# Kernel tuning notes

Hardware: AMD Instinct MI355X
Metric: run time of the kernel (lower is better)

The kernel has to match this reference:

```python
import jax, jax.numpy as jnp
import numpy as np

N_HEAD = 16
D_HEAD = 64
D_MODEL = 1024
LN_EPS = 1e-5


def layer_norm(x, gamma, beta):
    mu = jnp.mean(x, axis=-1, keepdims=True)
    var = jnp.mean((x - mu) ** 2, axis=-1, keepdims=True)
    return (x - mu) * jax.lax.rsqrt(var + LN_EPS) * gamma + beta


def setup_inputs() -> dict:
    key = jax.random.key(0)
    ks = jax.random.split(key, 6)
    B, T = 2, 2048
    inp = jax.random.normal(ks[0], (B, T, D_MODEL), dtype=jnp.float32)
    # qkv_net: Linear(d_model, 3*n_head*d_head)
    W_qkv = jax.random.normal(ks[1], (3 * N_HEAD * D_HEAD, D_MODEL), dtype=jnp.float32) * (D_MODEL ** -0.5)
    b_qkv = jax.random.normal(ks[2], (3 * N_HEAD * D_HEAD,), dtype=jnp.float32) * 0.02
    # o_net: Linear(n_head*d_head, d_model, bias=False)
    W_o = jax.random.normal(ks[3], (D_MODEL, N_HEAD * D_HEAD), dtype=jnp.float32) * ((N_HEAD * D_HEAD) ** -0.5)
    gamma = jnp.ones((D_MODEL,), dtype=jnp.float32)
    beta = jnp.zeros((D_MODEL,), dtype=jnp.float32)
    return {"inp": inp, "W_qkv": W_qkv, "b_qkv": b_qkv, "W_o": W_o, "gamma": gamma, "beta": beta}


def reference(inp, W_qkv, b_qkv, W_o, gamma, beta):
    B, T, D = inp.shape
    H, dh = N_HEAD, D_HEAD
    scale = 1.0 / (dh ** 0.5)

    qkv = inp @ W_qkv.T + b_qkv                      # (B, T, 3*H*dh)
    head_q, head_k, head_v = jnp.split(qkv, 3, axis=2)
    # (B, T, H, dh) -> (B, H, T, dh)
    q = head_q.reshape(B, T, H, dh).transpose(0, 2, 1, 3)
    k = head_k.reshape(B, T, H, dh).transpose(0, 2, 1, 3)
    v = head_v.reshape(B, T, H, dh).transpose(0, 2, 1, 3)

    attn_score = jnp.einsum('bhqd,bhkd->bhqk', q, k) * scale  # (B, H, T, T)
    attn_prob = jax.nn.softmax(attn_score, axis=-1)           # dropatt is identity in eval
    attn_vec = jnp.einsum('bhqk,bhkd->bhqd', attn_prob, v)    # (B, H, T, dh)

    # Faithful to original: (B*H, T, dh) batch-major buffer is VIEWED as (H, B, T, dh)
    attn_vec = attn_vec.reshape(H, B, T, dh)
    attn_vec = attn_vec.transpose(1, 2, 0, 3).reshape(B, T, H * dh)

    attn_out = attn_vec @ W_o.T                                # dropout identity in eval
    return layer_norm(inp + attn_out, gamma, beta)
```

## Files before the change

### kernel.cpp

```cpp
#include <hip/hip_runtime.h>
#include <hip/hip_bf16.h>
#include <stdint.h>

typedef __bf16 bf16_t;
typedef __bf16 bf16x8 __attribute__((ext_vector_type(8)));
typedef __bf16 bf16x4 __attribute__((ext_vector_type(4)));
typedef __bf16 bf16x2 __attribute__((ext_vector_type(2)));
typedef float floatx4 __attribute__((ext_vector_type(4)));

#define QSCALE 0.180336879f

#if __has_builtin(__builtin_amdgcn_cvt_pk_bf16_f32)
#define HAS_PK_BF16 1
#endif

__device__ static inline void gll16(const void* g, void* l) {
    __builtin_amdgcn_global_load_lds((const __attribute__((address_space(1))) void*)g,
                                     (__attribute__((address_space(3))) void*)l, 16, 0, 0);
}

__device__ static inline bf16x8 pack8(const float* p) {
    bf16x8 o;
#ifdef HAS_PK_BF16
#pragma unroll
    for (int j = 0; j < 4; j++) {
        bf16x2 t2 = __builtin_amdgcn_cvt_pk_bf16_f32(p[2 * j], p[2 * j + 1]);
        o[2 * j] = t2[0]; o[2 * j + 1] = t2[1];
    }
#else
#pragma unroll
    for (int j = 0; j < 8; j++) o[j] = (bf16_t)p[j];
#endif
    return o;
}

__global__ __launch_bounds__(256) void cvt_all(const float* __restrict__ inp,
                                               const float* __restrict__ wqkv,
                                               const float* __restrict__ wo,
                                               bf16_t* __restrict__ o_inp,
                                               bf16_t* __restrict__ o_wqkv,
                                               bf16_t* __restrict__ o_wo) {
    int blk = blockIdx.x;
    const float* src;
    bf16_t* dst;
    if (blk < 4096)      { src = inp;  dst = o_inp; }
    else if (blk < 7168) { src = wqkv; dst = o_wqkv; blk -= 4096; }
    else                 { src = wo;   dst = o_wo;   blk -= 7168; }
    int i = blk * 256 + threadIdx.x;
    float4 v = ((const float4*)src)[i];
    float p[4] = {v.x, v.y, v.z, v.w};
    bf16x4 o;
#ifdef HAS_PK_BF16
    bf16x2 t0 = __builtin_amdgcn_cvt_pk_bf16_f32(p[0], p[1]);
    bf16x2 t1 = __builtin_amdgcn_cvt_pk_bf16_f32(p[2], p[3]);
    o[0] = t0[0]; o[1] = t0[1]; o[2] = t1[0]; o[3] = t1[1];
#else
    o[0] = (bf16_t)p[0]; o[1] = (bf16_t)p[1]; o[2] = (bf16_t)p[2]; o[3] = (bf16_t)p[3];
#endif
    ((bf16x4*)dst)[i] = o;
}

__global__ __launch_bounds__(256, 3)
void gemm_qkv(const bf16_t* __restrict__ A, const bf16_t* __restrict__ Bw,
              const float* __restrict__ bias,
              bf16_t* __restrict__ qk, bf16_t* __restrict__ vT) {
    constexpr int K = 1024;
    __shared__ bf16_t lA[2][128 * 32];
    __shared__ bf16_t lB[2][128 * 32];
    const int tid  = threadIdx.x;
    const int lane = tid & 63, wave = tid >> 6;
    const int quad = lane >> 4, l16 = lane & 15;
    const int wy = wave >> 1, wx = wave & 1;
    const int bm = blockIdx.y * 128, bn = blockIdx.x * 128;

    const int c0 = tid, c1 = tid + 256;
    const bf16_t* Ap0 = A + (size_t)(bm + (c0 >> 2)) * K + (c0 & 3) * 8;
    const bf16_t* Ap1 = A + (size_t)(bm + (c1 >> 2)) * K + (c1 & 3) * 8;
    const bf16_t* Bp0 = Bw + (size_t)(bn + (c0 >> 2)) * K + (c0 & 3) * 8;
    const bf16_t* Bp1 = Bw + (size_t)(bn + (c1 >> 2)) * K + (c1 & 3) * 8;
    const int d0 = (wave * 64) * 8;
    const int d1 = (256 + wave * 64) * 8;

    floatx4 acc[4][4] = {};

    gll16(Ap0, &lA[0][d0]);
    gll16(Ap1, &lA[0][d1]);
    gll16(Bp0, &lB[0][d0]);
    gll16(Bp1, &lB[0][d1]);

    for (int it = 0; it < 32; ++it) {
        const int cur = it & 1, nxt = cur ^ 1;
        __syncthreads();
        if (it < 31) {
            const int kt = (it + 1) * 32;
            gll16(Ap0 + kt, &lA[nxt][d0]);
            gll16(Ap1 + kt, &lA[nxt][d1]);
            gll16(Bp0 + kt, &lB[nxt][d0]);
            gll16(Bp1 + kt, &lB[nxt][d1]);
        }
        bf16x8 af[4], bfr[4];
#pragma unroll
        for (int i = 0; i < 4; i++) {
            af[i]  = *(const bf16x8*)(&lA[cur][(wy * 64 + i * 16 + l16) * 32 + quad * 8]);
            bfr[i] = *(const bf16x8*)(&lB[cur][(wx * 64 + i * 16 + l16) * 32 + quad * 8]);
        }
#pragma unroll
        for (int i = 0; i < 4; i++)
#pragma unroll
            for (int j = 0; j < 4; j++)
                acc[i][j] = __builtin_amdgcn_mfma_f32_16x16x32_bf16(af[i], bfr[j], acc[i][j], 0, 0, 0);
    }

    const bool is_v = (bn >= 2048);
#pragma unroll
    for (int j = 0; j < 4; j++) {
        const int n = bn + wx * 64 + j * 16 + l16;
        const float bv = bias[n];
        const bool isq = (n < 1024);
#pragma unroll
        for (int i = 0; i < 4; i++) {
            const int mbase = bm + wy * 64 + i * 16 + quad * 4;
            if (!is_v) {
#pragma unroll
                for (int r = 0; r < 4; r++) {
                    float c = acc[i][j][r] + bv;
                    if (isq) c *= QSCALE;
                    qk[(size_t)(mbase + r) * 2048 + n] = (bf16_t)c;
                }
            } else {
                const int nn = n - 2048;
                const int b  = mbase >> 11;
                const int t  = mbase & 2047;
                const int vrow = b * 1024 + nn;
                const int pcol = (t & ~31) | (((t >> 2) & 3) << 3) | (((t >> 4) & 1) << 2);
                bf16x4 pack;
#pragma unroll
                for (int r = 0; r < 4; r++) pack[r] = (bf16_t)(acc[i][j][r] + bv);
                *(bf16x4*)(vT + (size_t)vrow * 2048 + pcol) = pack;
            }
        }
    }
}

__global__ __launch_bounds__(256, 4)
void attn_kernel(const bf16_t* __restrict__ qk, const bf16_t* __restrict__ vT,
                 bf16_t* __restrict__ Opart, float* __restrict__ lpart) {
    __shared__ bf16_t Kbuf[2][64 * 64];
    __shared__ bf16_t Vbuf[2][64 * 64];
    const int tid  = threadIdx.x;
    const int lane = tid & 63, wave = tid >> 6;
    const int quad = lane >> 4, l16 = lane & 15;
    const int bid = blockIdx.x;
    const int s    = bid & 63;
    const int hl   = ((s & 7) << 2) | ((s >> 3) & 3);
    const int half = (s >> 5) & 1;
    const int qt   = bid >> 6;
    const int b = hl >> 4, h = hl & 15;
    const int kt0 = half * 1024;

    const bf16_t* Qbase = qk + (size_t)(b * 2048 + qt * 128 + wave * 32) * 2048 + h * 64;
    const bf16_t* Kbase = qk + (size_t)(b * 2048) * 2048 + 1024 + h * 64;
    const bf16_t* Vbase = vT + (size_t)(hl * 64) * 2048;

    const int srow = tid >> 2, sc8 = (tid & 3) * 8;
    const bf16_t* KgA = Kbase + (size_t)(kt0 + srow) * 2048 + sc8;
    const bf16_t* KgB = KgA + 32;
    const bf16_t* VgA = Vbase + (size_t)srow * 2048 + kt0 + sc8;
    const bf16_t* VgB = VgA + 32;
    const int wbase = wave * 512;

    bf16x8 qf[2][2];
#pragma unroll
    for (int rt = 0; rt < 2; rt++)
#pragma unroll
        for (int kc = 0; kc < 2; kc++)
            qf[rt][kc] = *(const bf16x8*)(Qbase + (size_t)(rt * 16 + l16) * 2048 + kc * 32 + quad * 8);

    floatx4 accO[2][4] = {};
    float lacc[2] = {0.f, 0.f};

    gll16(KgA, &Kbuf[0][wbase]);
    gll16(KgB, &Kbuf[0][2048 + wbase]);
    gll16(VgA, &Vbuf[0][wbase]);
    gll16(VgB, &Vbuf[0][2048 + wbase]);

    for (int it = 0; it < 16; ++it) {
        const int cur = it & 1, nxt = cur ^ 1;
        __syncthreads();
        if (it < 15) {
            const size_t ko = (size_t)(it + 1) * 64 * 2048;
            const int    vo = (it + 1) * 64;
            gll16(KgA + ko, &Kbuf[nxt][wbase]);
            gll16(KgB + ko, &Kbuf[nxt][2048 + wbase]);
            gll16(VgA + vo, &Vbuf[nxt][wbase]);
            gll16(VgB + vo, &Vbuf[nxt][2048 + wbase]);
        }
        floatx4 st[2][4] = {};
#pragma unroll
        for (int nt = 0; nt < 4; nt++) {
            bf16x8 k0 = *(const bf16x8*)&Kbuf[cur][(nt * 16 + l16) * 32 + quad * 8];
            bf16x8 k1 = *(const bf16x8*)&Kbuf[cur][2048 + (nt * 16 + l16) * 32 + quad * 8];
            st[0][nt] = __builtin_amdgcn_mfma_f32_16x16x32_bf16(k0, qf[0][0], st[0][nt], 0, 0, 0);
            st[0][nt] = __builtin_amdgcn_mfma_f32_16x16x32_bf16(k1, qf[0][1], st[0][nt], 0, 0, 0);
            st[1][nt] = __builtin_amdgcn_mfma_f32_16x16x32_bf16(k0, qf[1][0], st[1][nt], 0, 0, 0);
            st[1][nt] = __builtin_amdgcn_mfma_f32_16x16x32_bf16(k1, qf[1][1], st[1][nt], 0, 0, 0);
        }
#pragma unroll
        for (int kc2 = 0; kc2 < 2; kc2++) {
            bf16x8 vf[4];
#pragma unroll
            for (int ct = 0; ct < 4; ct++)
                vf[ct] = *(const bf16x8*)&Vbuf[cur][kc2 * 2048 + (ct * 16 + l16) * 32 + quad * 8];
#pragma unroll
            for (int rt = 0; rt < 2; rt++) {
                float p[8];
                float ls = 0.f;
#pragma unroll
                for (int j = 0; j < 8; j++) {
                    p[j] = __builtin_amdgcn_exp2f(st[rt][kc2 * 2 + (j >> 2)][j & 3]);
                    ls += p[j];
                }
                lacc[rt] += ls;
                bf16x8 pf = pack8(p);
#pragma unroll
                for (int ct = 0; ct < 4; ct++)
                    accO[rt][ct] = __builtin_amdgcn_mfma_f32_16x16x32_bf16(pf, vf[ct], accO[rt][ct], 0, 0, 0);
            }
        }
    }

    float lsum[2];
#pragma unroll
    for (int rt = 0; rt < 2; rt++) {
        float l = lacc[rt];
        l += __shfl_xor(l, 16);
        l += __shfl_xor(l, 32);
        lsum[rt] = l;
    }
    const int b2 = hl & 1;
    const int colb = hl >> 1;
    const int rowb = b2 * 2048 + qt * 128 + wave * 32;
    bf16_t* outb = Opart + (size_t)half * (4096 * 1024) + (size_t)rowb * 1024 + colb * 64;
#pragma unroll
    for (int rt = 0; rt < 2; rt++)
#pragma unroll
        for (int ct = 0; ct < 4; ct++)
#pragma unroll
            for (int r = 0; r < 4; r++)
                outb[(size_t)(rt * 16 + quad * 4 + r) * 1024 + ct * 16 + l16] = (bf16_t)(accO[rt][ct][r]);
    if (quad == 0) {
#pragma unroll
        for (int rt = 0; rt < 2; rt++)
            lpart[half * 65536 + (rowb + rt * 16 + l16) * 16 + colb] = lsum[rt];
    }
}

__global__ __launch_bounds__(256, 4)
void gemm_o(const bf16_t* __restrict__ Op, const float* __restrict__ lp,
            const bf16_t* __restrict__ Bw, bf16_t* __restrict__ out) {
    constexpr int K = 1024;
    __shared__ bf16_t lA[2][64 * 32];
    __shared__ bf16_t lB[2][128 * 32];
    const int tid  = threadIdx.x;
    const int lane = tid & 63, wave = tid >> 6;
    const int quad = lane >> 4, l16 = lane & 15;
    const int wy = wave >> 1, wx = wave & 1;
    const int bm = blockIdx.y * 64, bn = blockIdx.x * 128;

    const int ca = tid;
    const int arow = bm + (ca >> 2);
    const int ak   = (ca & 3) * 8;
    const bf16_t* Ap0 = Op + (size_t)arow * 1024 + ak;
    const bf16_t* Ap1 = Ap0 + (size_t)4096 * 1024;
    const float*  lrow = lp + arow * 16;
    const int cb0 = tid, cb1 = tid + 256;
    const bf16_t* Bp0 = Bw + (size_t)(bn + (cb0 >> 2)) * K + (cb0 & 3) * 8;
    const bf16_t* Bp1 = Bw + (size_t)(bn + (cb1 >> 2)) * K + (cb1 & 3) * 8;
    const int d0 = (wave * 64) * 8;
    const int d1 = (256 + wave * 64) * 8;

    gll16(Bp0, &lB[0][d0]);
    gll16(Bp1, &lB[0][d1]);
    {
        bf16x8 a0 = *(const bf16x8*)(Ap0);
        bf16x8 a1 = *(const bf16x8*)(Ap1);
        const float inv = 1.0f / (lrow[ak >> 6] + lrow[65536 + (ak >> 6)]);
        float p[8];
#pragma unroll
        for (int j = 0; j < 8; j++) p[j] = ((float)a0[j] + (float)a1[j]) * inv;
        *(bf16x8*)&lA[0][ca * 8] = pack8(p);
    }

    floatx4 acc[2][4] = {};
    for (int it = 0; it < 32; ++it) {
        const int cur = it & 1, nxt = cur ^ 1;
        __syncthreads();
        bf16x8 na0, na1;
        int kt1 = (it + 1) * 32;
        if (it < 31) {
            na0 = *(const bf16x8*)(Ap0 + kt1);
            na1 = *(const bf16x8*)(Ap1 + kt1);
            gll16(Bp0 + kt1, &lB[nxt][d0]);
            gll16(Bp1 + kt1, &lB[nxt][d1]);
        }
        bf16x8 af[2], bfr[4];
#pragma unroll
        for (int i = 0; i < 2; i++)
            af[i] = *(const bf16x8*)(&lA[cur][(wy * 32 + i * 16 + l16) * 32 + quad * 8]);
#pragma unroll
        for (int j = 0; j < 4; j++)
            bfr[j] = *(const bf16x8*)(&lB[cur][(wx * 64 + j * 16 + l16) * 32 + quad * 8]);
#pragma unroll
        for (int i = 0; i < 2; i++)
#pragma unroll
            for (int j = 0; j < 4; j++)
                acc[i][j] = __builtin_amdgcn_mfma_f32_16x16x32_bf16(af[i], bfr[j], acc[i][j], 0, 0, 0);
        if (it < 31) {
            const int cb = (kt1 + ak) >> 6;
            const float inv = 1.0f / (lrow[cb] + lrow[65536 + cb]);
            float p[8];
#pragma unroll
            for (int j = 0; j < 8; j++) p[j] = ((float)na0[j] + (float)na1[j]) * inv;
            *(bf16x8*)&lA[nxt][ca * 8] = pack8(p);
        }
    }
#pragma unroll
    for (int j = 0; j < 4; j++) {
        const int n = bn + wx * 64 + j * 16 + l16;
#pragma unroll
        for (int i = 0; i < 2; i++) {
            const int mbase = bm + wy * 32 + i * 16 + quad * 4;
#pragma unroll
            for (int r = 0; r < 4; r++)
                out[(size_t)(mbase + r) * 1024 + n] = (bf16_t)acc[i][j][r];
        }
    }
}

__global__ __launch_bounds__(256)
void ln_kernel(const float* __restrict__ inp, const bf16_t* __restrict__ ao,
               const float* __restrict__ gamma, const float* __restrict__ beta,
               float* __restrict__ out) {
    const int row = blockIdx.x, tid = threadIdx.x;
    const int wave = tid >> 6, lane = tid & 63;
    float4 a = ((const float4*)(inp + (size_t)row * 1024))[tid];
    bf16x4 c4 = ((const bf16x4*)(ao + (size_t)row * 1024))[tid];
    float x0 = a.x + (float)c4[0], x1 = a.y + (float)c4[1];
    float x2 = a.z + (float)c4[2], x3 = a.w + (float)c4[3];
    float s = x0 + x1 + x2 + x3;
    float sq = x0 * x0 + x1 * x1 + x2 * x2 + x3 * x3;
#pragma unroll
    for (int mm = 32; mm >= 1; mm >>= 1) {
        s += __shfl_xor(s, mm);
        sq += __shfl_xor(sq, mm);
    }
    __shared__ float rs[4], rq[4];
    if (lane == 0) { rs[wave] = s; rq[wave] = sq; }
    __syncthreads();
    s = rs[0] + rs[1] + rs[2] + rs[3];
    sq = rq[0] + rq[1] + rq[2] + rq[3];
    const float mu = s * (1.0f / 1024.0f);
    const float var = sq * (1.0f / 1024.0f) - mu * mu;
    const float rstd = rsqrtf(var + 1e-5f);
    float4 g = ((const float4*)gamma)[tid], bt = ((const float4*)beta)[tid];
    float4 o;
    o.x = (x0 - mu) * rstd * g.x + bt.x;
    o.y = (x1 - mu) * rstd * g.y + bt.y;
    o.z = (x2 - mu) * rstd * g.z + bt.z;
    o.w = (x3 - mu) * rstd * g.w + bt.w;
    ((float4*)(out + (size_t)row * 1024))[tid] = o;
}

extern "C" void kernel_launch(void* const* d_in, const int* in_sizes, int n_in,
                              void* d_out, int out_size, void* d_ws, size_t ws_size,
                              hipStream_t stream) {
    const float* inp   = (const float*)d_in[0];
    const float* Wqkv  = (const float*)d_in[1];
    const float* bqkv  = (const float*)d_in[2];
    const float* Wo    = (const float*)d_in[3];
    const float* gamma = (const float*)d_in[4];
    const float* beta  = (const float*)d_in[5];
    float* out = (float*)d_out;

    char* ws = (char*)d_ws;
    bf16_t* inp_bf  = (bf16_t*)(ws);
    bf16_t* wqkv_bf = (bf16_t*)(ws + (8u << 20));
    bf16_t* wo_bf   = (bf16_t*)(ws + (14u << 20));
    bf16_t* qk_buf  = (bf16_t*)(ws + (16u << 20));
    bf16_t* vT_buf  = (bf16_t*)(ws + (32u << 20));
    bf16_t* ao_bf   = (bf16_t*)(ws + (32u << 20));
    bf16_t* opart   = (bf16_t*)(ws + (48u << 20));
    float*  lpart   = (float*)(ws);

    cvt_all<<<8192, 256, 0, stream>>>(inp, Wqkv, Wo, inp_bf, wqkv_bf, wo_bf);
    gemm_qkv<<<dim3(24, 32), 256, 0, stream>>>(inp_bf, wqkv_bf, bqkv, qk_buf, vT_buf);
    attn_kernel<<<1024, 256, 0, stream>>>(qk_buf, vT_buf, opart, lpart);
    gemm_o<<<dim3(8, 64), 256, 0, stream>>>(opart, lpart, wo_bf, ao_bf);
    ln_kernel<<<4096, 256, 0, stream>>>(inp, ao_bf, gamma, beta, out);
}
```

Before: 202.0 us.

## Shrink attention tiles to 16 query rows per wave and 32-key steps

Each attention block now covers 64 query rows instead of 128, with one 16-row tile per wave, and streams K/V in 32-key chunks over 32 iterations. The grid doubles to 2048 blocks and launch bounds target 8 blocks per CU. The row sum of P is now computed by an MFMA against a ones vector instead of scalar adds and shuffles. This cuts LDS and register use to raise occupancy, but halves reuse of each loaded K/V tile, so global/LDS traffic per FLOP rises and there are more barriers.

```diff
diff --git a/kernel.cpp b/kernel.cpp
--- a/kernel.cpp
+++ b/kernel.cpp
@@ -142,11 +142,11 @@
     }
 }
 
-__global__ __launch_bounds__(256, 4)
+__global__ __launch_bounds__(256, 8)
 void attn_kernel(const bf16_t* __restrict__ qk, const bf16_t* __restrict__ vT,
                  bf16_t* __restrict__ Opart, float* __restrict__ lpart) {
-    __shared__ bf16_t Kbuf[2][64 * 64];
-    __shared__ bf16_t Vbuf[2][64 * 64];
+    __shared__ bf16_t Kbuf[2][2][32 * 32];
+    __shared__ bf16_t Vbuf[2][64 * 32];
     const int tid  = threadIdx.x;
     const int lane = tid & 63, wave = tid >> 6;
     const int quad = lane >> 4, l16 = lane & 15;
@@ -158,100 +158,76 @@
     const int b = hl >> 4, h = hl & 15;
     const int kt0 = half * 1024;
 
-    const bf16_t* Qbase = qk + (size_t)(b * 2048 + qt * 128 + wave * 32) * 2048 + h * 64;
+    const bf16_t* Qbase = qk + (size_t)(b * 2048 + qt * 64 + wave * 16) * 2048 + h * 64;
     const bf16_t* Kbase = qk + (size_t)(b * 2048) * 2048 + 1024 + h * 64;
     const bf16_t* Vbase = vT + (size_t)(hl * 64) * 2048;
 
-    const int srow = tid >> 2, sc8 = (tid & 3) * 8;
-    const bf16_t* KgA = Kbase + (size_t)(kt0 + srow) * 2048 + sc8;
-    const bf16_t* KgB = KgA + 32;
-    const bf16_t* VgA = Vbase + (size_t)srow * 2048 + kt0 + sc8;
-    const bf16_t* VgB = VgA + 32;
-    const int wbase = wave * 512;
-
-    bf16x8 qf[2][2];
-#pragma unroll
-    for (int rt = 0; rt < 2; rt++)
-#pragma unroll
-        for (int kc = 0; kc < 2; kc++)
-            qf[rt][kc] = *(const bf16x8*)(Qbase + (size_t)(rt * 16 + l16) * 2048 + kc * 32 + quad * 8);
-
-    floatx4 accO[2][4] = {};
-    float lacc[2] = {0.f, 0.f};
-
-    gll16(KgA, &Kbuf[0][wbase]);
-    gll16(KgB, &Kbuf[0][2048 + wbase]);
-    gll16(VgA, &Vbuf[0][wbase]);
-    gll16(VgB, &Vbuf[0][2048 + wbase]);
-
-    for (int it = 0; it < 16; ++it) {
+    const int khalf = tid >> 7;
+    const int kt_r  = (tid & 127) >> 2;
+    const int kd    = (tid & 3) * 8;
+    const bf16_t* Kg = Kbase + (size_t)(kt0 + kt_r) * 2048 + khalf * 32 + kd;
+    const int vd = tid >> 2;
+    const int vp = (tid & 3) * 8;
+    const bf16_t* Vg = Vbase + (size_t)vd * 2048 + kt0 + vp;
+    const int kdst = (wave & 1) * 512;
+    const int vdst = wave * 512;
+
+    bf16x8 qf[2];
+#pragma unroll
+    for (int kc = 0; kc < 2; kc++)
+        qf[kc] = *(const bf16x8*)(Qbase + (size_t)l16 * 2048 + kc * 32 + quad * 8);
+
+    bf16x8 ones;
+#pragma unroll
+    for (int j = 0; j < 8; j++) ones[j] = (bf16_t)1.0f;
+
+    floatx4 accO[4] = {};
+    floatx4 acc_l = {};
+
+    gll16(Kg, &Kbuf[0][khalf][kdst]);
+    gll16(Vg, &Vbuf[0][vdst]);
+
+    for (int it = 0; it < 32; ++it) {
         const int cur = it & 1, nxt = cur ^ 1;
         __syncthreads();
-        if (it < 15) {
-            const size_t ko = (size_t)(it + 1) * 64 * 2048;
-            const int    vo = (it + 1) * 64;
-            gll16(KgA + ko, &Kbuf[nxt][wbase]);
-            gll16(KgB + ko, &Kbuf[nxt][2048 + wbase]);
-            gll16(VgA + vo, &Vbuf[nxt][wbase]);
-            gll16(VgB + vo, &Vbuf[nxt][2048 + wbase]);
-        }
-        floatx4 st[2][4] = {};
-#pragma unroll
-        for (int nt = 0; nt < 4; nt++) {
-            bf16x8 k0 = *(const bf16x8*)&Kbuf[cur][(nt * 16 + l16) * 32 + quad * 8];
-            bf16x8 k1 = *(const bf16x8*)&Kbuf[cur][2048 + (nt * 16 + l16) * 32 + quad * 8];
-            st[0][nt] = __builtin_amdgcn_mfma_f32_16x16x32_bf16(k0, qf[0][0], st[0][nt], 0, 0, 0);
-            st[0][nt] = __builtin_amdgcn_mfma_f32_16x16x32_bf16(k1, qf[0][1], st[0][nt], 0, 0, 0);
-            st[1][nt] = __builtin_amdgcn_mfma_f32_16x16x32_bf16(k0, qf[1][0], st[1][nt], 0, 0, 0);
-            st[1][nt] = __builtin_amdgcn_mfma_f32_16x16x32_bf16(k1, qf[1][1], st[1][nt], 0, 0, 0);
-        }
-#pragma unroll
-        for (int kc2 = 0; kc2 < 2; kc2++) {
-            bf16x8 vf[4];
-#pragma unroll
-            for (int ct = 0; ct < 4; ct++)
-                vf[ct] = *(const bf16x8*)&Vbuf[cur][kc2 * 2048 + (ct * 16 + l16) * 32 + quad * 8];
-#pragma unroll
-            for (int rt = 0; rt < 2; rt++) {
-                float p[8];
-                float ls = 0.f;
-#pragma unroll
-                for (int j = 0; j < 8; j++) {
-                    p[j] = __builtin_amdgcn_exp2f(st[rt][kc2 * 2 + (j >> 2)][j & 3]);
-                    ls += p[j];
-                }
-                lacc[rt] += ls;
-                bf16x8 pf = pack8(p);
-#pragma unroll
-                for (int ct = 0; ct < 4; ct++)
-                    accO[rt][ct] = __builtin_amdgcn_mfma_f32_16x16x32_bf16(pf, vf[ct], accO[rt][ct], 0, 0, 0);
-            }
-        }
-    }
-
-    float lsum[2];
-#pragma unroll
-    for (int rt = 0; rt < 2; rt++) {
-        float l = lacc[rt];
-        l += __shfl_xor(l, 16);
-        l += __shfl_xor(l, 32);
-        lsum[rt] = l;
-    }
+        if (it < 31) {
+            gll16(Kg + (size_t)(it + 1) * 32 * 2048, &Kbuf[nxt][khalf][kdst]);
+            gll16(Vg + (it + 1) * 32, &Vbuf[nxt][vdst]);
+        }
+        floatx4 st[2] = {};
+#pragma unroll
+        for (int nt = 0; nt < 2; nt++) {
+            bf16x8 k0 = *(const bf16x8*)&Kbuf[cur][0][(nt * 16 + l16) * 32 + quad * 8];
+            bf16x8 k1 = *(const bf16x8*)&Kbuf[cur][1][(nt * 16 + l16) * 32 + quad * 8];
+            st[nt] = __builtin_amdgcn_mfma_f32_16x16x32_bf16(k0, qf[0], st[nt], 0, 0, 0);
+            st[nt] = __builtin_amdgcn_mfma_f32_16x16x32_bf16(k1, qf[1], st[nt], 0, 0, 0);
+        }
+        float p[8];
+#pragma unroll
+        for (int j = 0; j < 8; j++)
+            p[j] = __builtin_amdgcn_exp2f(st[j >> 2][j & 3]);
+        bf16x8 pf = pack8(p);
+        acc_l = __builtin_amdgcn_mfma_f32_16x16x32_bf16(pf, ones, acc_l, 0, 0, 0);
+#pragma unroll
+        for (int ct = 0; ct < 4; ct++) {
+            bf16x8 vf = *(const bf16x8*)&Vbuf[cur][(ct * 16 + l16) * 32 + quad * 8];
+            accO[ct] = __builtin_amdgcn_mfma_f32_16x16x32_bf16(pf, vf, accO[ct], 0, 0, 0);
+        }
+    }
+
     const int b2 = hl & 1;
     const int colb = hl >> 1;
-    const int rowb = b2 * 2048 + qt * 128 + wave * 32;
+    const int rowb = b2 * 2048 + qt * 64 + wave * 16;
     bf16_t* outb = Opart + (size_t)half * (4096 * 1024) + (size_t)rowb * 1024 + colb * 64;
 #pragma unroll
-    for (int rt = 0; rt < 2; rt++)
-#pragma unroll
-        for (int ct = 0; ct < 4; ct++)
-#pragma unroll
-            for (int r = 0; r < 4; r++)
-                outb[(size_t)(rt * 16 + quad * 4 + r) * 1024 + ct * 16 + l16] = (bf16_t)(accO[rt][ct][r]);
-    if (quad == 0) {
-#pragma unroll
-        for (int rt = 0; rt < 2; rt++)
-            lpart[half * 65536 + (rowb + rt * 16 + l16) * 16 + colb] = lsum[rt];
+    for (int ct = 0; ct < 4; ct++)
+#pragma unroll
+        for (int r = 0; r < 4; r++)
+            outb[(size_t)(quad * 4 + r) * 1024 + ct * 16 + l16] = (bf16_t)(accO[ct][r]);
+    if (l16 == 0) {
+#pragma unroll
+        for (int r = 0; r < 4; r++)
+            lpart[half * 65536 + (rowb + quad * 4 + r) * 16 + colb] = acc_l[r];
     }
 }
 
@@ -394,7 +370,7 @@
 
     cvt_all<<<8192, 256, 0, stream>>>(inp, Wqkv, Wo, inp_bf, wqkv_bf, wo_bf);
     gemm_qkv<<<dim3(24, 32), 256, 0, stream>>>(inp_bf, wqkv_bf, bqkv, qk_buf, vT_buf);
-    attn_kernel<<<1024, 256, 0, stream>>>(qk_buf, vT_buf, opart, lpart);
+    attn_kernel<<<2048, 256, 0, stream>>>(qk_buf, vT_buf, opart, lpart);
     gemm_o<<<dim3(8, 64), 256, 0, stream>>>(opart, lpart, wo_bf, ao_bf);
     ln_kernel<<<4096, 256, 0, stream>>>(inp, ao_bf, gamma, beta, out);
 }
```

Result: slower. 207.9 us (+2.9%).
